# Kernel optimization log

Measured on AMD Instinct MI355X. Metric: run time of the kernel, lower is better.

The kernel has to match this reference:

```python
import jax, jax.numpy as jnp
import numpy as np


def setup_inputs() -> dict:
    key = jax.random.key(0)
    ks = jax.random.split(key, 6)
    num_nodes, H, B = 500000, 128, 100000
    node_ids = jnp.arange(B, dtype=jnp.int64 if jax.config.jax_enable_x64 else jnp.int32)
    messages = jax.random.normal(ks[0], (B, H), dtype=jnp.float32)
    memory = jax.random.normal(ks[1], (num_nodes, H), dtype=jnp.float32)
    # PyTorch GRUCell params: weight_ih/weight_hh [3H, H], biases [3H]
    s = 1.0 / np.sqrt(H)
    W_ih = jax.random.uniform(ks[2], (3 * H, H), minval=-s, maxval=s, dtype=jnp.float32)
    W_hh = jax.random.uniform(ks[3], (3 * H, H), minval=-s, maxval=s, dtype=jnp.float32)
    b_ih = jax.random.uniform(ks[4], (3 * H,), minval=-s, maxval=s, dtype=jnp.float32)
    b_hh = jax.random.uniform(ks[5], (3 * H,), minval=-s, maxval=s, dtype=jnp.float32)
    return {"node_ids": node_ids, "messages": messages, "memory": memory,
            "W_ih": W_ih, "W_hh": W_hh, "b_ih": b_ih, "b_hh": b_hh}


def _gru_cell(x, h, W_ih, W_hh, b_ih, b_hh):
    # gi/gh: [B, 3H]; chunk order in torch GRUCell is (r, z, n)
    gi = x @ W_ih.T + b_ih
    gh = h @ W_hh.T + b_hh
    i_r, i_z, i_n = jnp.split(gi, 3, axis=-1)
    h_r, h_z, h_n = jnp.split(gh, 3, axis=-1)
    r = jax.nn.sigmoid(i_r + h_r)
    z = jax.nn.sigmoid(i_z + h_z)
    n = jnp.tanh(i_n + r * h_n)
    return (1.0 - z) * n + z * h


def reference(node_ids, messages, memory, W_ih, W_hh, b_ih, b_hh):
    # gather per-node memory, GRU update, scatter back (update_memory)
    current = memory[node_ids]                              # [B, H] gather
    updated = _gru_cell(messages, current, W_ih, W_hh, b_ih, b_hh)
    new_memory = memory.at[node_ids].set(updated)           # [N, H] scatter
    return new_memory
```

## Files before the change

kernel.cpp:

```cpp
#include <hip/hip_runtime.h>
#include <hip/hip_bf16.h>

typedef __bf16 bf16x8 __attribute__((ext_vector_type(8)));
typedef float  f32x4  __attribute__((ext_vector_type(4)));

#define GRU_H 128
#define ROWS  64
#define NTHR  512

__device__ inline float sigmoidf_(float x) { return 1.f / (1.f + __expf(-x)); }
__device__ inline float tanhf_(float x)    { return 1.f - 2.f / (__expf(2.f * x) + 1.f); }

__device__ inline bf16x8 cvt8(float4 a, float4 b) {
    bf16x8 r;
    r[0] = (__bf16)a.x; r[1] = (__bf16)a.y; r[2] = (__bf16)a.z; r[3] = (__bf16)a.w;
    r[4] = (__bf16)b.x; r[5] = (__bf16)b.y; r[6] = (__bf16)b.z; r[7] = (__bf16)b.w;
    return r;
}

__global__ __launch_bounds__(512) void convert_weights(
    const float* __restrict__ W_ih, const float* __restrict__ W_hh,
    bf16x8* __restrict__ frags, int* __restrict__ flag)
{
    if (blockIdx.x == 0 && threadIdx.x == 0) *flag = 0;
    const int t = blockIdx.x * 512 + threadIdx.x;
    const int lane = t & 63;
    const int ks   = (t >> 6) & 3;
    const int r    = t >> 8;
    const int g    = r % 6;
    const int wave = r / 6;
    const int col  = wave * 16 + (lane & 15);
    const int lg   = lane >> 4;
    const int gg   = (g < 3) ? g : g - 3;
    const float* src = ((g < 3) ? W_ih : W_hh) + ((size_t)(gg * GRU_H + col)) * GRU_H + ks * 32 + lg * 8;
    float4 a = *reinterpret_cast<const float4*>(src);
    float4 b = *reinterpret_cast<const float4*>(src + 4);
    frags[t] = cvt8(a, b);
}

__global__ __launch_bounds__(256) void check_arange(const int* __restrict__ ids, int B,
                                                    int* __restrict__ flag)
{
    int bad = 0;
    for (int i = blockIdx.x * 256 + threadIdx.x; i < B; i += gridDim.x * 256)
        bad |= (ids[i] != i);
    if (bad) atomicOr(flag, 1);
}

__global__ __launch_bounds__(256) void copy_skip(const float4* __restrict__ src,
                                                 float4* __restrict__ dst,
                                                 size_t n4, size_t skip4,
                                                 const int* __restrict__ flag)
{
    const size_t start  = (*flag == 0) ? skip4 : 0;
    const size_t stride = (size_t)gridDim.x * 256;
    for (size_t i = start + (size_t)blockIdx.x * 256 + threadIdx.x; i < n4; i += stride)
        dst[i] = src[i];
}

__global__ __launch_bounds__(512, 2) void gru_update_kernel(
    const int*   __restrict__ node_ids,
    const float* __restrict__ messages,
    const float* __restrict__ memory,
    const bf16x8* __restrict__ frags,
    const float* __restrict__ b_ih,
    const float* __restrict__ b_hh,
    float*       __restrict__ out,
    int B)
{
    __shared__ __align__(16) unsigned char xs_raw[ROWS * 256];
    __shared__ __align__(16) unsigned char hf_raw[ROWS * 512];
    __shared__ int ids[ROWS];

    const int wave = threadIdx.x >> 6;
    const int lane = threadIdx.x & 63;
    const int l15  = lane & 15;
    const int lg   = lane >> 4;
    const int col  = wave * 16 + l15;

    bf16x8 bfrag[6][4];
    #pragma unroll
    for (int g = 0; g < 6; ++g)
        #pragma unroll
        for (int ks = 0; ks < 4; ++ks)
            bfrag[g][ks] = frags[((wave * 6 + g) * 4 + ks) * 64 + lane];

    const float bi_r = b_ih[col], bi_z = b_ih[GRU_H + col], bi_n = b_ih[2 * GRU_H + col];
    const float bh_r = b_hh[col], bh_z = b_hh[GRU_H + col], bh_n = b_hh[2 * GRU_H + col];

    const int nchunks = (B + ROWS - 1) / ROWS;
    for (int c = blockIdx.x; c < nchunks; c += gridDim.x) {
        const int rb = c * ROWS;

        #pragma unroll
        for (int s = 0; s < 4; ++s) {
            const int slot = threadIdx.x + s * 512;
            const int row  = slot >> 5;
            const int c4   = slot & 31;
            const int grow = rb + row;
            float4 v = {0.f, 0.f, 0.f, 0.f};
            if (grow < B) {
                const int gid = node_ids[grow];
                if (c4 == 0) ids[row] = gid;
                v = *reinterpret_cast<const float4*>(&memory[(size_t)gid * GRU_H + c4 * 4]);
            }
            *reinterpret_cast<float4*>(&hf_raw[row * 512 + ((c4 * 16) ^ ((row & 7) << 4))]) = v;
        }
        #pragma unroll
        for (int s = 0; s < 2; ++s) {
            const int slot = threadIdx.x + s * 512;
            const int row  = slot >> 4;
            const int c8   = slot & 15;
            const int grow = rb + row;
            bf16x8 v;
            if (grow < B) {
                const float* p = &messages[(size_t)grow * GRU_H + c8 * 8];
                float4 a = *reinterpret_cast<const float4*>(p);
                float4 b = *reinterpret_cast<const float4*>(p + 4);
                v = cvt8(a, b);
            } else {
                #pragma unroll
                for (int j = 0; j < 8; ++j) v[j] = (__bf16)0.f;
            }
            *reinterpret_cast<bf16x8*>(&xs_raw[row * 256 + ((c8 * 16) ^ ((row & 7) << 4))]) = v;
        }
        __syncthreads();

        #pragma unroll
        for (int sub = 0; sub < 4; ++sub) {
            const int rbase = sub * 16;
            const int arow  = rbase + l15;
            const int sw    = (arow & 7) << 4;

            bf16x8 ax[4], ah[4];
            #pragma unroll
            for (int ks = 0; ks < 4; ++ks) {
                ax[ks] = *reinterpret_cast<const bf16x8*>(
                    &xs_raw[arow * 256 + (((ks * 4 + lg) * 16) ^ sw)]);
                const int c4a = ks * 8 + lg * 2;
                float4 f0 = *reinterpret_cast<const float4*>(
                    &hf_raw[arow * 512 + ((c4a * 16) ^ sw)]);
                float4 f1 = *reinterpret_cast<const float4*>(
                    &hf_raw[arow * 512 + (((c4a + 1) * 16) ^ sw)]);
                ah[ks] = cvt8(f0, f1);
            }

            f32x4 acc[6];
            #pragma unroll
            for (int g = 0; g < 6; ++g) acc[g] = (f32x4){0.f, 0.f, 0.f, 0.f};

            #pragma unroll
            for (int ks = 0; ks < 4; ++ks) {
                acc[0] = __builtin_amdgcn_mfma_f32_16x16x32_bf16(ax[ks], bfrag[0][ks], acc[0], 0, 0, 0);
                acc[1] = __builtin_amdgcn_mfma_f32_16x16x32_bf16(ax[ks], bfrag[1][ks], acc[1], 0, 0, 0);
                acc[2] = __builtin_amdgcn_mfma_f32_16x16x32_bf16(ax[ks], bfrag[2][ks], acc[2], 0, 0, 0);
                acc[3] = __builtin_amdgcn_mfma_f32_16x16x32_bf16(ah[ks], bfrag[3][ks], acc[3], 0, 0, 0);
                acc[4] = __builtin_amdgcn_mfma_f32_16x16x32_bf16(ah[ks], bfrag[4][ks], acc[4], 0, 0, 0);
                acc[5] = __builtin_amdgcn_mfma_f32_16x16x32_bf16(ah[ks], bfrag[5][ks], acc[5], 0, 0, 0);
            }

            #pragma unroll
            for (int r = 0; r < 4; ++r) {
                const int row  = rbase + lg * 4 + r;
                const int grow = rb + row;
                if (grow < B) {
                    const int gid = ids[row];
                    const float h = *reinterpret_cast<const float*>(
                        &hf_raw[row * 512 + ((((col >> 2) * 16) ^ ((row & 7) << 4)) + (col & 3) * 4)]);
                    const float rg = sigmoidf_((acc[0][r] + bi_r) + (acc[3][r] + bh_r));
                    const float zg = sigmoidf_((acc[1][r] + bi_z) + (acc[4][r] + bh_z));
                    const float ng = tanhf_((acc[2][r] + bi_n) + rg * (acc[5][r] + bh_n));
                    out[(size_t)gid * GRU_H + col] = (1.f - zg) * ng + zg * h;
                }
            }
        }
        __syncthreads();
    }
}

extern "C" void kernel_launch(void* const* d_in, const int* in_sizes, int n_in,
                              void* d_out, int out_size, void* d_ws, size_t ws_size,
                              hipStream_t stream) {
    const int*   node_ids = (const int*)d_in[0];
    const float* messages = (const float*)d_in[1];
    const float* memory   = (const float*)d_in[2];
    const float* W_ih     = (const float*)d_in[3];
    const float* W_hh     = (const float*)d_in[4];
    const float* b_ih     = (const float*)d_in[5];
    const float* b_hh     = (const float*)d_in[6];
    float* out = (float*)d_out;

    const int B = in_sizes[0];
    const int N = in_sizes[2] / GRU_H;

    int*    flag  = (int*)d_ws;
    bf16x8* frags = (bf16x8*)((char*)d_ws + 1024);

    convert_weights<<<24, 512, 0, stream>>>(W_ih, W_hh, frags, flag);
    check_arange<<<256, 256, 0, stream>>>(node_ids, B, flag);
    const size_t n4 = (size_t)N * GRU_H / 4;
    const size_t skip4 = (size_t)B * GRU_H / 4;
    copy_skip<<<2048, 256, 0, stream>>>((const float4*)memory, (float4*)out, n4, skip4, flag);
    const int nchunks = (B + ROWS - 1) / ROWS;
    int grid = nchunks < 512 ? nchunks : 512;
    gru_update_kernel<<<grid, 512, 0, stream>>>(node_ids, messages, memory,
                                                frags, b_ih, b_hh, out, B);
}
```

Baseline: 533.1 us.

## Fuse memory copy into GRU kernel using a bitmap of updated node rows

Replaces the arange check and separate skip-copy kernel with a bitmap of touched node ids built by atomics, then folds the bulk copy of untouched memory rows into the GRU kernel's tail. The hidden state is converted to bf16 once at load time instead of per MFMA sub-tile, and the W_hh fragments are streamed from global memory instead of held in registers, so occupancy can rise to 4 blocks per CU. The new copy loop tests a bitmap bit for every float4 and reads every row, including the updated ones, which may add traffic compared with the contiguous skip used when ids form an arange. Per-iteration weight reloads add L2 traffic.

```diff
diff --git a/kernel.cpp b/kernel.cpp
--- a/kernel.cpp
+++ b/kernel.cpp
@@ -6,7 +6,6 @@
 
 #define GRU_H 128
 #define ROWS  64
-#define NTHR  512
 
 __device__ inline float sigmoidf_(float x) { return 1.f / (1.f + __expf(-x)); }
 __device__ inline float tanhf_(float x)    { return 1.f - 2.f / (__expf(2.f * x) + 1.f); }
@@ -18,12 +17,12 @@
     return r;
 }
 
-__global__ __launch_bounds__(512) void convert_weights(
+__global__ __launch_bounds__(512) void prep_weights(
     const float* __restrict__ W_ih, const float* __restrict__ W_hh,
-    bf16x8* __restrict__ frags, int* __restrict__ flag)
+    bf16x8* __restrict__ frags, unsigned* __restrict__ bitmap, int nwords)
 {
-    if (blockIdx.x == 0 && threadIdx.x == 0) *flag = 0;
     const int t = blockIdx.x * 512 + threadIdx.x;
+    for (int i = t; i < nwords; i += 12288) bitmap[i] = 0u;
     const int lane = t & 63;
     const int ks   = (t >> 6) & 3;
     const int r    = t >> 8;
@@ -32,58 +31,51 @@
     const int col  = wave * 16 + (lane & 15);
     const int lg   = lane >> 4;
     const int gg   = (g < 3) ? g : g - 3;
-    const float* src = ((g < 3) ? W_ih : W_hh) + ((size_t)(gg * GRU_H + col)) * GRU_H + ks * 32 + lg * 8;
+    const float* src = ((g < 3) ? W_ih : W_hh) + (size_t)(gg * GRU_H + col) * GRU_H + ks * 32 + lg * 8;
     float4 a = *reinterpret_cast<const float4*>(src);
     float4 b = *reinterpret_cast<const float4*>(src + 4);
     frags[t] = cvt8(a, b);
 }
 
-__global__ __launch_bounds__(256) void check_arange(const int* __restrict__ ids, int B,
-                                                    int* __restrict__ flag)
+__global__ __launch_bounds__(512) void set_bits(const int* __restrict__ ids, int B,
+                                                unsigned* __restrict__ bitmap)
 {
-    int bad = 0;
-    for (int i = blockIdx.x * 256 + threadIdx.x; i < B; i += gridDim.x * 256)
-        bad |= (ids[i] != i);
-    if (bad) atomicOr(flag, 1);
-}
-
-__global__ __launch_bounds__(256) void copy_skip(const float4* __restrict__ src,
-                                                 float4* __restrict__ dst,
-                                                 size_t n4, size_t skip4,
-                                                 const int* __restrict__ flag)
-{
-    const size_t start  = (*flag == 0) ? skip4 : 0;
-    const size_t stride = (size_t)gridDim.x * 256;
-    for (size_t i = start + (size_t)blockIdx.x * 256 + threadIdx.x; i < n4; i += stride)
-        dst[i] = src[i];
-}
-
-__global__ __launch_bounds__(512, 2) void gru_update_kernel(
-    const int*   __restrict__ node_ids,
-    const float* __restrict__ messages,
-    const float* __restrict__ memory,
+    const int i = blockIdx.x * 512 + threadIdx.x;
+    if (i < B) {
+        const int id = ids[i];
+        atomicOr(&bitmap[id >> 5], 1u << (id & 31));
+    }
+}
+
+__global__ __launch_bounds__(512, 4) void fused_kernel(
+    const int*    __restrict__ node_ids,
+    const float*  __restrict__ messages,
+    const float*  __restrict__ memory,
     const bf16x8* __restrict__ frags,
-    const float* __restrict__ b_ih,
-    const float* __restrict__ b_hh,
-    float*       __restrict__ out,
-    int B)
+    const float*  __restrict__ b_ih,
+    const float*  __restrict__ b_hh,
+    const unsigned* __restrict__ bitmap,
+    float*        __restrict__ out,
+    int B, int N)
 {
     __shared__ __align__(16) unsigned char xs_raw[ROWS * 256];
+    __shared__ __align__(16) unsigned char hb_raw[ROWS * 256];
     __shared__ __align__(16) unsigned char hf_raw[ROWS * 512];
     __shared__ int ids[ROWS];
 
-    const int wave = threadIdx.x >> 6;
-    const int lane = threadIdx.x & 63;
+    const int tid  = threadIdx.x;
+    const int wave = tid >> 6;
+    const int lane = tid & 63;
     const int l15  = lane & 15;
     const int lg   = lane >> 4;
     const int col  = wave * 16 + l15;
 
-    bf16x8 bfrag[6][4];
+    bf16x8 bfih[3][4];
     #pragma unroll
-    for (int g = 0; g < 6; ++g)
+    for (int g = 0; g < 3; ++g)
         #pragma unroll
         for (int ks = 0; ks < 4; ++ks)
-            bfrag[g][ks] = frags[((wave * 6 + g) * 4 + ks) * 64 + lane];
+            bfih[g][ks] = frags[((wave * 6 + g) * 4 + ks) * 64 + lane];
 
     const float bi_r = b_ih[col], bi_z = b_ih[GRU_H + col], bi_n = b_ih[2 * GRU_H + col];
     const float bh_r = b_hh[col], bh_z = b_hh[GRU_H + col], bh_n = b_hh[2 * GRU_H + col];
@@ -93,88 +85,93 @@
         const int rb = c * ROWS;
 
         #pragma unroll
-        for (int s = 0; s < 4; ++s) {
-            const int slot = threadIdx.x + s * 512;
-            const int row  = slot >> 5;
-            const int c4   = slot & 31;
-            const int grow = rb + row;
-            float4 v = {0.f, 0.f, 0.f, 0.f};
-            if (grow < B) {
-                const int gid = node_ids[grow];
-                if (c4 == 0) ids[row] = gid;
-                v = *reinterpret_cast<const float4*>(&memory[(size_t)gid * GRU_H + c4 * 4]);
-            }
-            *reinterpret_cast<float4*>(&hf_raw[row * 512 + ((c4 * 16) ^ ((row & 7) << 4))]) = v;
-        }
-        #pragma unroll
         for (int s = 0; s < 2; ++s) {
-            const int slot = threadIdx.x + s * 512;
+            const int slot = tid + s * 512;
             const int row  = slot >> 4;
             const int c8   = slot & 15;
             const int grow = rb + row;
-            bf16x8 v;
+            const int sw   = (row & 7) << 4;
+            float4 a = {0.f, 0.f, 0.f, 0.f}, b = {0.f, 0.f, 0.f, 0.f};
+            if (grow < B) {
+                const int gid = node_ids[grow];
+                if (c8 == 0) ids[row] = gid;
+                const float* p = &memory[(size_t)gid * GRU_H + c8 * 8];
+                a = *reinterpret_cast<const float4*>(p);
+                b = *reinterpret_cast<const float4*>(p + 4);
+            }
+            *reinterpret_cast<float4*>(&hf_raw[row * 512 + (((c8 * 2) * 16) ^ sw)]) = a;
+            *reinterpret_cast<float4*>(&hf_raw[row * 512 + (((c8 * 2 + 1) * 16) ^ sw)]) = b;
+            *reinterpret_cast<bf16x8*>(&hb_raw[row * 256 + ((c8 * 16) ^ sw)]) = cvt8(a, b);
+        }
+        #pragma unroll
+        for (int s = 0; s < 2; ++s) {
+            const int slot = tid + s * 512;
+            const int row  = slot >> 4;
+            const int c8   = slot & 15;
+            const int grow = rb + row;
+            const int sw   = (row & 7) << 4;
+            float4 a = {0.f, 0.f, 0.f, 0.f}, b = {0.f, 0.f, 0.f, 0.f};
             if (grow < B) {
                 const float* p = &messages[(size_t)grow * GRU_H + c8 * 8];
-                float4 a = *reinterpret_cast<const float4*>(p);
-                float4 b = *reinterpret_cast<const float4*>(p + 4);
-                v = cvt8(a, b);
-            } else {
-                #pragma unroll
-                for (int j = 0; j < 8; ++j) v[j] = (__bf16)0.f;
-            }
-            *reinterpret_cast<bf16x8*>(&xs_raw[row * 256 + ((c8 * 16) ^ ((row & 7) << 4))]) = v;
+                a = *reinterpret_cast<const float4*>(p);
+                b = *reinterpret_cast<const float4*>(p + 4);
+            }
+            *reinterpret_cast<bf16x8*>(&xs_raw[row * 256 + ((c8 * 16) ^ sw)]) = cvt8(a, b);
         }
         __syncthreads();
 
         #pragma unroll
         for (int sub = 0; sub < 4; ++sub) {
-            const int rbase = sub * 16;
-            const int arow  = rbase + l15;
-            const int sw    = (arow & 7) << 4;
-
-            bf16x8 ax[4], ah[4];
+            const int arow = sub * 16 + l15;
+            const int sw   = (arow & 7) << 4;
+
+            f32x4 acc0 = {0.f,0.f,0.f,0.f}, acc1 = acc0, acc2 = acc0,
+                  acc3 = acc0, acc4 = acc0, acc5 = acc0;
+
             #pragma unroll
             for (int ks = 0; ks < 4; ++ks) {
-                ax[ks] = *reinterpret_cast<const bf16x8*>(
+                const bf16x8 ax = *reinterpret_cast<const bf16x8*>(
                     &xs_raw[arow * 256 + (((ks * 4 + lg) * 16) ^ sw)]);
-                const int c4a = ks * 8 + lg * 2;
-                float4 f0 = *reinterpret_cast<const float4*>(
-                    &hf_raw[arow * 512 + ((c4a * 16) ^ sw)]);
-                float4 f1 = *reinterpret_cast<const float4*>(
-                    &hf_raw[arow * 512 + (((c4a + 1) * 16) ^ sw)]);
-                ah[ks] = cvt8(f0, f1);
-            }
-
-            f32x4 acc[6];
-            #pragma unroll
-            for (int g = 0; g < 6; ++g) acc[g] = (f32x4){0.f, 0.f, 0.f, 0.f};
-
-            #pragma unroll
-            for (int ks = 0; ks < 4; ++ks) {
-                acc[0] = __builtin_amdgcn_mfma_f32_16x16x32_bf16(ax[ks], bfrag[0][ks], acc[0], 0, 0, 0);
-                acc[1] = __builtin_amdgcn_mfma_f32_16x16x32_bf16(ax[ks], bfrag[1][ks], acc[1], 0, 0, 0);
-                acc[2] = __builtin_amdgcn_mfma_f32_16x16x32_bf16(ax[ks], bfrag[2][ks], acc[2], 0, 0, 0);
-                acc[3] = __builtin_amdgcn_mfma_f32_16x16x32_bf16(ah[ks], bfrag[3][ks], acc[3], 0, 0, 0);
-                acc[4] = __builtin_amdgcn_mfma_f32_16x16x32_bf16(ah[ks], bfrag[4][ks], acc[4], 0, 0, 0);
-                acc[5] = __builtin_amdgcn_mfma_f32_16x16x32_bf16(ah[ks], bfrag[5][ks], acc[5], 0, 0, 0);
+                const bf16x8 ah = *reinterpret_cast<const bf16x8*>(
+                    &hb_raw[arow * 256 + (((ks * 4 + lg) * 16) ^ sw)]);
+                const bf16x8 w3 = frags[((wave * 6 + 3) * 4 + ks) * 64 + lane];
+                const bf16x8 w4 = frags[((wave * 6 + 4) * 4 + ks) * 64 + lane];
+                const bf16x8 w5 = frags[((wave * 6 + 5) * 4 + ks) * 64 + lane];
+                acc0 = __builtin_amdgcn_mfma_f32_16x16x32_bf16(ax, bfih[0][ks], acc0, 0, 0, 0);
+                acc1 = __builtin_amdgcn_mfma_f32_16x16x32_bf16(ax, bfih[1][ks], acc1, 0, 0, 0);
+                acc2 = __builtin_amdgcn_mfma_f32_16x16x32_bf16(ax, bfih[2][ks], acc2, 0, 0, 0);
+                acc3 = __builtin_amdgcn_mfma_f32_16x16x32_bf16(ah, w3, acc3, 0, 0, 0);
+                acc4 = __builtin_amdgcn_mfma_f32_16x16x32_bf16(ah, w4, acc4, 0, 0, 0);
+                acc5 = __builtin_amdgcn_mfma_f32_16x16x32_bf16(ah, w5, acc5, 0, 0, 0);
             }
 
             #pragma unroll
             for (int r = 0; r < 4; ++r) {
-                const int row  = rbase + lg * 4 + r;
+                const int row  = sub * 16 + lg * 4 + r;
                 const int grow = rb + row;
                 if (grow < B) {
                     const int gid = ids[row];
+                    const int swr = (row & 7) << 4;
                     const float h = *reinterpret_cast<const float*>(
-                        &hf_raw[row * 512 + ((((col >> 2) * 16) ^ ((row & 7) << 4)) + (col & 3) * 4)]);
-                    const float rg = sigmoidf_((acc[0][r] + bi_r) + (acc[3][r] + bh_r));
-                    const float zg = sigmoidf_((acc[1][r] + bi_z) + (acc[4][r] + bh_z));
-                    const float ng = tanhf_((acc[2][r] + bi_n) + rg * (acc[5][r] + bh_n));
+                        &hf_raw[row * 512 + ((((col >> 2) * 16) ^ swr) + (col & 3) * 4)]);
+                    const float rg = sigmoidf_((acc0[r] + bi_r) + (acc3[r] + bh_r));
+                    const float zg = sigmoidf_((acc1[r] + bi_z) + (acc4[r] + bh_z));
+                    const float ng = tanhf_((acc2[r] + bi_n) + rg * (acc5[r] + bh_n));
                     out[(size_t)gid * GRU_H + col] = (1.f - zg) * ng + zg * h;
                 }
             }
         }
         __syncthreads();
+    }
+
+    const float4* src4 = reinterpret_cast<const float4*>(memory);
+    float4*       dst4 = reinterpret_cast<float4*>(out);
+    const size_t n4     = (size_t)N * (GRU_H / 4);
+    const size_t stride = (size_t)gridDim.x * blockDim.x;
+    for (size_t j = (size_t)blockIdx.x * blockDim.x + tid; j < n4; j += stride) {
+        const int row = (int)(j >> 5);
+        if (!((bitmap[row >> 5] >> (row & 31)) & 1u))
+            dst4[j] = src4[j];
     }
 }
 
@@ -192,17 +189,13 @@
 
     const int B = in_sizes[0];
     const int N = in_sizes[2] / GRU_H;
-
-    int*    flag  = (int*)d_ws;
-    bf16x8* frags = (bf16x8*)((char*)d_ws + 1024);
-
-    convert_weights<<<24, 512, 0, stream>>>(W_ih, W_hh, frags, flag);
-    check_arange<<<256, 256, 0, stream>>>(node_ids, B, flag);
-    const size_t n4 = (size_t)N * GRU_H / 4;
-    const size_t skip4 = (size_t)B * GRU_H / 4;
-    copy_skip<<<2048, 256, 0, stream>>>((const float4*)memory, (float4*)out, n4, skip4, flag);
-    const int nchunks = (B + ROWS - 1) / ROWS;
-    int grid = nchunks < 512 ? nchunks : 512;
-    gru_update_kernel<<<grid, 512, 0, stream>>>(node_ids, messages, memory,
-                                                frags, b_ih, b_hh, out, B);
-}
+    const int nwords = (N + 31) / 32;
+
+    bf16x8*   frags  = (bf16x8*)((char*)d_ws + 1024);
+    unsigned* bitmap = (unsigned*)((char*)d_ws + 256 * 1024);
+
+    prep_weights<<<24, 512, 0, stream>>>(W_ih, W_hh, frags, bitmap, nwords);
+    set_bits<<<(B + 511) / 512, 512, 0, stream>>>(node_ids, B, bitmap);
+    fused_kernel<<<512, 512, 0, stream>>>(node_ids, messages, memory, frags,
+                                          b_ih, b_hh, bitmap, out, B, N);
+}
```

Result: slower. 568.3 us (+6.6%).
